# Kernel optimization log

Hardware: AMD Instinct MI355X
Metric: run time of the kernel (lower is better)

The kernel has to match this reference:

```python
import jax, jax.numpy as jnp
import numpy as np

N_NODES = 262144
N_EDGES = 4194304
N_GRAPHS = 1024


def setup_inputs() -> dict:
    key = jax.random.key(0)
    ks = jax.random.split(key, 12)
    inp = {}
    inp["x"] = jax.random.normal(ks[0], (N_NODES, 4), dtype=jnp.float32)
    inp["pos"] = jax.random.normal(ks[1], (N_NODES, 3), dtype=jnp.float32)
    # EquiLayer MLP: Linear(9,16) -> SiLU -> Linear(16,16); stored as (in,out)
    inp["W1"] = jax.random.normal(ks[2], (9, 16), dtype=jnp.float32) * (1.0 / np.sqrt(9))
    inp["b1"] = jnp.zeros((16,), dtype=jnp.float32)
    inp["W2"] = jax.random.normal(ks[3], (16, 16), dtype=jnp.float32) * 0.25
    inp["b2"] = jnp.zeros((16,), dtype=jnp.float32)
    # pool: Linear(16, k=2)
    inp["Wp"] = jax.random.normal(ks[4], (16, 2), dtype=jnp.float32) * 0.25
    inp["bp"] = jnp.zeros((2,), dtype=jnp.float32)
    # to_z: Linear(k*16=32, k*d=8)
    inp["Wz"] = jax.random.normal(ks[5], (32, 8), dtype=jnp.float32) * (1.0 / np.sqrt(32))
    inp["bz"] = jnp.zeros((8,), dtype=jnp.float32)
    inp["edge_index"] = jax.random.randint(ks[6], (2, N_EDGES), 0, N_NODES, dtype=jnp.int64)
    inp["batch"] = jnp.sort(jax.random.randint(ks[7], (N_NODES,), 0, N_GRAPHS, dtype=jnp.int64))
    return inp


def reference(x, pos, W1, b1, W2, b2, Wp, bp, Wz, bz, edge_index, batch):
    src = edge_index[0]  # x_j / source nodes
    dst = edge_index[1]  # x_i / target nodes (aggregation index, PyG default flow)
    n = x.shape[0]
    g = N_GRAPHS

    # edge distance feature: ||pos[src] - pos[dst]||  -> [E,1]
    rel = pos[src] - pos[dst]
    dist = jnp.sqrt(jnp.sum(rel * rel, axis=-1, keepdims=True))

    # message MLP on gathered endpoints: concat([x_i, x_j, dist]) -> [E,9]
    m_in = jnp.concatenate([x[dst], x[src], dist], axis=-1)
    h1 = jax.nn.silu(m_in @ W1 + b1)
    msg = h1 @ W2 + b2  # [E,16]

    # scatter-mean aggregation over target nodes
    msum = jax.ops.segment_sum(msg, dst, num_segments=n)
    cnt = jax.ops.segment_sum(jnp.ones((msg.shape[0], 1), msg.dtype), dst, num_segments=n)
    agg = msum / jnp.maximum(cnt, 1.0)

    h = jax.nn.relu(agg)  # [N,16]
    s = jax.nn.softmax(h @ Wp + bp, axis=-1)  # [N,k]

    # softmax-weighted scatter-sum pooling per graph: [G,k,16]
    pooled = jax.ops.segment_sum(s[:, :, None] * h[:, None, :], batch, num_segments=g)
    z = pooled.reshape(g, -1) @ Wz + bz  # [G, k*d]
    return z, s
```

## Files before the change

kernel.cpp:

```cpp
#include <hip/hip_runtime.h>
#include <hip/hip_fp16.h>
#include <math.h>

#define N_NODES 262144
#define N_EDGES 4194304
#define N_GRAPHS 1024
#define NBK 512
#define CAP 8960
#define ABLK 512
#define AEPB (N_EDGES / ABLK)

typedef _Float16 half2v __attribute__((ext_vector_type(2)));
__device__ inline half2v u2h(unsigned u) { union { unsigned u; half2v h; } c; c.u = u; return c.h; }
__device__ inline unsigned packh2(float a, float b) {
    union { __half2 h; unsigned u; } c; c.h = __floats2half2_rn(a, b); return c.u;
}

__global__ __launch_bounds__(256) void fusedAB(
    const int* __restrict__ ei, const float* __restrict__ x,
    const float* __restrict__ pos, int* __restrict__ gcur,
    int* __restrict__ binned, uint4* __restrict__ px16,
    float* __restrict__ pooled)
{
    __shared__ int lh2[2][NBK];
    int t = threadIdx.x, b = blockIdx.x;
    int half = (t >> 6) & 1;

    #pragma unroll
    for (int k = 0; k < 2; ++k) {
        int n = b * 512 + k * 256 + t;
        float4 v = ((const float4*)x)[n];
        float p0 = pos[3 * n], p1 = pos[3 * n + 1], p2 = pos[3 * n + 2];
        uint4 r;
        r.x = packh2(v.x, v.y);
        r.y = packh2(v.z, v.w);
        r.z = packh2(p0, p1);
        r.w = packh2(p2, 0.0f);
        px16[n] = r;
    }
    int pid = b * 256 + t;
    if (pid < 1025 * 32) pooled[pid] = 0.0f;

    #pragma unroll
    for (int k = 0; k < 2; ++k) {
        lh2[0][t + 256 * k] = 0;
        lh2[1][t + 256 * k] = 0;
    }
    __syncthreads();

    const int4* dsts = (const int4*)(ei + N_EDGES + b * AEPB);
    #pragma unroll
    for (int i = 0; i < AEPB / 1024; ++i) {
        int4 d4 = dsts[i * 256 + t];
        atomicAdd(&lh2[half][d4.x >> 9], 1);
        atomicAdd(&lh2[half][d4.y >> 9], 1);
        atomicAdd(&lh2[half][d4.z >> 9], 1);
        atomicAdd(&lh2[half][d4.w >> 9], 1);
    }
    __syncthreads();
    #pragma unroll
    for (int k = 0; k < 2; ++k) {
        int kb = t + 256 * k;
        int tot = lh2[0][kb] + lh2[1][kb];
        lh2[0][kb] = atomicAdd(&gcur[kb * 16], tot);
    }
    __syncthreads();
    const int4* srcp = (const int4*)(ei + b * AEPB);
    #pragma unroll
    for (int i = 0; i < AEPB / 1024; ++i) {
        int4 s4 = srcp[i * 256 + t];
        int4 d4 = dsts[i * 256 + t];
        int slot;
        slot = atomicAdd(&lh2[0][d4.x >> 9], 1);
        if (slot < CAP) binned[(size_t)(d4.x >> 9) * CAP + slot] = s4.x | ((d4.x & 511) << 18);
        slot = atomicAdd(&lh2[0][d4.y >> 9], 1);
        if (slot < CAP) binned[(size_t)(d4.y >> 9) * CAP + slot] = s4.y | ((d4.y & 511) << 18);
        slot = atomicAdd(&lh2[0][d4.z >> 9], 1);
        if (slot < CAP) binned[(size_t)(d4.z >> 9) * CAP + slot] = s4.z | ((d4.z & 511) << 18);
        slot = atomicAdd(&lh2[0][d4.w >> 9], 1);
        if (slot < CAP) binned[(size_t)(d4.w >> 9) * CAP + slot] = s4.w | ((d4.w & 511) << 18);
    }
}

__global__ __launch_bounds__(512) void passC_sort(
    const int* __restrict__ gcur,
    int* __restrict__ binned,
    int4* __restrict__ ndesc)
{
    __shared__ int lbuf[CAP];
    __shared__ int ldeg[512], lcur[512];
    __shared__ int wsum[8];
    int t = threadIdx.x, k = blockIdx.x;
    int ebase = k * CAP;
    int cnt = gcur[k * 16];
    if (cnt > CAP) cnt = CAP;

    ldeg[t] = 0;
    __syncthreads();
    for (int i = t; i < cnt; i += 512) {
        int pk = binned[ebase + i];
        lbuf[i] = pk;
        atomicAdd(&ldeg[pk >> 18], 1);
    }
    __syncthreads();
    int dgv = ldeg[t];

    int lane = t & 63, wid = t >> 6;
    int sv = dgv;
    #pragma unroll
    for (int o = 1; o < 64; o <<= 1) {
        int u = __shfl_up(sv, o);
        if (lane >= o) sv += u;
    }
    if (lane == 63) wsum[wid] = sv;
    __syncthreads();
    int pref = 0;
    #pragma unroll
    for (int w = 0; w < 8; ++w) pref += (w < wid) ? wsum[w] : 0;
    int excl = sv + pref - dgv;

    int n = k * 512 + t;
    lcur[t] = excl;

    int wbase = t & ~15;
    int rank = 0;
    #pragma unroll
    for (int j = 0; j < 16; ++j) {
        int dj = ldeg[wbase + j];
        rank += (dj < dgv) || (dj == dgv && (wbase + j) < t);
    }
    ndesc[(k << 9) + wbase + rank] = make_int4(ebase + excl, dgv, n, 0);
    __syncthreads();
    for (int i = t; i < cnt; i += 512) {
        int pk = lbuf[i];
        int sl = atomicAdd(&lcur[pk >> 18], 1);
        binned[ebase + sl] = pk & 0x3FFFF;
    }
}

__global__ __launch_bounds__(256) void node_gather_fused(
    const uint4* __restrict__ px16,
    const int* __restrict__ srcs, const int4* __restrict__ ndesc,
    const float* __restrict__ W1, const float* __restrict__ b1,
    const float* __restrict__ W2, const float* __restrict__ b2,
    const float* __restrict__ Wp, const float* __restrict__ bp,
    const int* __restrict__ batch,
    float* __restrict__ out_s, float* __restrict__ pooled)
{
    __shared__ uint4 sepk[16][17];
    __shared__ float smh[16][20];

    int t = threadIdx.x;
    int g = t & 15;
    int grp = t >> 4;
    int4 nd = ndesc[blockIdx.x * 16 + grp];
    int base = nd.x, dg = nd.y, n = nd.z;

    float w1c0 = W1[0 * 16 + g], w1c1 = W1[1 * 16 + g];
    float w1c2 = W1[2 * 16 + g], w1c3 = W1[3 * 16 + g];
    half2v wh45, wh67;
    wh45[0] = (_Float16)W1[4 * 16 + g];
    wh45[1] = (_Float16)W1[5 * 16 + g];
    wh67[0] = (_Float16)W1[6 * 16 + g];
    wh67[1] = (_Float16)W1[7 * 16 + g];
    float w1c8 = W1[8 * 16 + g];
    float b1g = b1[g], b2g = b2[g];
    float w2col[16];
    #pragma unroll
    for (int i = 0; i < 16; ++i) w2col[i] = W2[i * 16 + g];
    float wp0 = Wp[2 * g], wp1 = Wp[2 * g + 1];

    uint4 rn = px16[n];
    float2 f01 = __half22float2(*(__half2*)&rn.x);
    float2 f23 = __half22float2(*(__half2*)&rn.y);
    float2 f45 = __half22float2(*(__half2*)&rn.z);
    float2 f67 = __half22float2(*(__half2*)&rn.w);
    float pnx = f45.x, pny = f45.y, pnz = f67.x;
    float pre = b1g + f01.x * w1c0 + f01.y * w1c1 + f23.x * w1c2 + f23.y * w1c3;

    float sumH = 0.0f;

    int sC = 0, sN, sNN;
    if (g < dg) sC = srcs[base + g];
    sN = sC;
    if (16 + g < dg) sN = srcs[base + 16 + g];
    sNN = sN;
    if (32 + g < dg) sNN = srcs[base + 32 + g];
    uint4 rC = px16[sC];
    uint4 rN = px16[sN];

    for (int k0 = 0; k0 < dg; k0 += 16) {
        int rem = dg - k0;
        int cnt = rem < 16 ? rem : 16;
        if (g < cnt) {
            float2 e45 = __half22float2(*(__half2*)&rC.z);
            float2 e67 = __half22float2(*(__half2*)&rC.w);
            float dx = e45.x - pnx, dy = e45.y - pny, dz = e67.x - pnz;
            float dist = sqrtf(dx * dx + dy * dy + dz * dz);
            sepk[grp][g] = make_uint4(rC.x, rC.y, __float_as_uint(dist), 0u);
        }
        uint4 rNN = px16[sNN];
        int sNNN = sNN;
        if (k0 + 48 + g < dg) sNNN = srcs[base + k0 + 48 + g];
        int j = 0;
        for (; j + 1 < cnt; j += 2) {
            uint4 A = sepk[grp][j];
            uint4 B = sepk[grp][j + 1];
            float a = fmaf(__uint_as_float(A.z), w1c8, pre);
            a = __builtin_amdgcn_fdot2(u2h(A.x), wh45, a, false);
            a = __builtin_amdgcn_fdot2(u2h(A.y), wh67, a, false);
            sumH += a * __builtin_amdgcn_rcpf(1.0f + __expf(-a));
            float b = fmaf(__uint_as_float(B.z), w1c8, pre);
            b = __builtin_amdgcn_fdot2(u2h(B.x), wh45, b, false);
            b = __builtin_amdgcn_fdot2(u2h(B.y), wh67, b, false);
            sumH += b * __builtin_amdgcn_rcpf(1.0f + __expf(-b));
        }
        if (j < cnt) {
            uint4 A = sepk[grp][j];
            float a = fmaf(__uint_as_float(A.z), w1c8, pre);
            a = __builtin_amdgcn_fdot2(u2h(A.x), wh45, a, false);
            a = __builtin_amdgcn_fdot2(u2h(A.y), wh67, a, false);
            sumH += a * __builtin_amdgcn_rcpf(1.0f + __expf(-a));
        }
        rC = rN; rN = rNN; sNN = sNNN;
    }

    smh[grp][g] = sumH;
    float4 s0v = *(const float4*)&smh[grp][0];
    float4 s1v = *(const float4*)&smh[grp][4];
    float4 s2v = *(const float4*)&smh[grp][8];
    float4 s3v = *(const float4*)&smh[grp][12];
    float red = s0v.x * w2col[0] + s0v.y * w2col[1] + s0v.z * w2col[2] + s0v.w * w2col[3]
              + s1v.x * w2col[4] + s1v.y * w2col[5] + s1v.z * w2col[6] + s1v.w * w2col[7]
              + s2v.x * w2col[8] + s2v.y * w2col[9] + s2v.z * w2col[10] + s2v.w * w2col[11]
              + s3v.x * w2col[12] + s3v.y * w2col[13] + s3v.z * w2col[14] + s3v.w * w2col[15];

    float fdg = (float)dg;
    float inv = 1.0f / fmaxf(fdg, 1.0f);
    float h = fmaxf((red + fdg * b2g) * inv, 0.0f);

    float c0 = h * wp0, c1 = h * wp1;
    #pragma unroll
    for (int mset = 8; mset > 0; mset >>= 1) {
        c0 += __shfl_xor(c0, mset);
        c1 += __shfl_xor(c1, mset);
    }
    float l0 = c0 + bp[0], l1 = c1 + bp[1];
    float mx = fmaxf(l0, l1);
    float e0s = __expf(l0 - mx), e1s = __expf(l1 - mx);
    float isum = 1.0f / (e0s + e1s);
    float s0 = e0s * isum, s1 = e1s * isum;

    if (g == 0) ((float2*)out_s)[n] = make_float2(s0, s1);

    __shared__ float lpool[2][32];
    __shared__ int sg0;
    if (t == 0) sg0 = batch[blockIdx.x * 16];
    if (t < 64) lpool[t >> 5][t & 31] = 0.0f;
    __syncthreads();

    int gid = batch[n];
    int idx = gid - sg0;
    float p0 = s0 * h, p1 = s1 * h;
    if (idx < 2) {
        atomicAdd(&lpool[idx][g], p0);
        atomicAdd(&lpool[idx][16 + g], p1);
    } else {
        atomicAdd(&pooled[gid * 32 + g], p0);
        atomicAdd(&pooled[gid * 32 + 16 + g], p1);
    }
    __syncthreads();
    if (t < 32) {
        float v = lpool[0][t];
        if (v != 0.0f) atomicAdd(&pooled[sg0 * 32 + t], v);
        v = lpool[1][t];
        if (v != 0.0f) atomicAdd(&pooled[(sg0 + 1) * 32 + t], v);
    }
}

__global__ __launch_bounds__(256) void z_kernel(const float* __restrict__ pooled,
                                                const float* __restrict__ Wz,
                                                const float* __restrict__ bz,
                                                float* __restrict__ out_z) {
    int idx = blockIdx.x * 256 + threadIdx.x;
    if (idx >= N_GRAPHS * 8) return;
    int gph = idx >> 3, o = idx & 7;
    float a = bz[o];
    const float* pp = pooled + (size_t)gph * 32;
    #pragma unroll
    for (int j = 0; j < 32; ++j) a = fmaf(pp[j], Wz[j * 8 + o], a);
    out_z[idx] = a;
}

extern "C" void kernel_launch(void* const* d_in, const int* in_sizes, int n_in,
                              void* d_out, int out_size, void* d_ws, size_t ws_size,
                              hipStream_t stream) {
    const float* x    = (const float*)d_in[0];
    const float* pos  = (const float*)d_in[1];
    const float* W1   = (const float*)d_in[2];
    const float* b1   = (const float*)d_in[3];
    const float* W2   = (const float*)d_in[4];
    const float* b2   = (const float*)d_in[5];
    const float* Wp   = (const float*)d_in[6];
    const float* bp   = (const float*)d_in[7];
    const float* Wz   = (const float*)d_in[8];
    const float* bz   = (const float*)d_in[9];
    const int*   ei   = (const int*)d_in[10];
    const int*   batch= (const int*)d_in[11];
    float* out = (float*)d_out;
    float* out_z = out;
    float* out_s = out + N_GRAPHS * 8;

    int* gcur     = (int*)d_ws;
    int* binned   = gcur + NBK * 16;
    int4* ndesc   = (int4*)(binned + (size_t)NBK * CAP);
    float* pooled = (float*)(ndesc + N_NODES);
    uint4* px16   = (uint4*)(pooled + 1025 * 32);

    hipMemsetAsync(gcur, 0, NBK * 16 * sizeof(int), stream);
    fusedAB<<<ABLK, 256, 0, stream>>>(ei, x, pos, gcur, binned, px16, pooled);
    passC_sort<<<NBK, 512, 0, stream>>>(gcur, binned, ndesc);
    node_gather_fused<<<N_NODES / 16, 256, 0, stream>>>(
        px16, binned, ndesc, W1, b1, W2, b2, Wp, bp, batch, out_s, pooled);
    z_kernel<<<32, 256, 0, stream>>>(pooled, Wz, bz, out_z);
}
```

Before: 173.9 us.

## Fuse bucket sort and node gather into one per-bucket kernel using LDS

Merges the per-bucket counting sort and the per-node message/aggregation kernel into a single kernel with one block per 512-node bucket. The sorted source lists, offsets, degree permutation and batch ids stay in shared memory, so the global write-back of sorted sources, the ndesc array and one launch are dropped. Each 16-lane group now processes 16 nodes in sequence, and graph pooling is reduced locally over up to 8 graphs per block. In exchange there are only 512 blocks with large LDS use (~50KB), which lowers occupancy and latency hiding for the random px16 gathers, and the prefetch depth drops from two chunks ahead to one.

```diff
diff --git a/kernel.cpp b/kernel.cpp
--- a/kernel.cpp
+++ b/kernel.cpp
@@ -82,79 +82,85 @@
     }
 }
 
-__global__ __launch_bounds__(512) void passC_sort(
-    const int* __restrict__ gcur,
-    int* __restrict__ binned,
-    int4* __restrict__ ndesc)
-{
-    __shared__ int lbuf[CAP];
-    __shared__ int ldeg[512], lcur[512];
-    __shared__ int wsum[8];
-    int t = threadIdx.x, k = blockIdx.x;
-    int ebase = k * CAP;
-    int cnt = gcur[k * 16];
-    if (cnt > CAP) cnt = CAP;
-
-    ldeg[t] = 0;
-    __syncthreads();
-    for (int i = t; i < cnt; i += 512) {
-        int pk = binned[ebase + i];
-        lbuf[i] = pk;
-        atomicAdd(&ldeg[pk >> 18], 1);
-    }
-    __syncthreads();
-    int dgv = ldeg[t];
-
-    int lane = t & 63, wid = t >> 6;
-    int sv = dgv;
-    #pragma unroll
-    for (int o = 1; o < 64; o <<= 1) {
-        int u = __shfl_up(sv, o);
-        if (lane >= o) sv += u;
-    }
-    if (lane == 63) wsum[wid] = sv;
-    __syncthreads();
-    int pref = 0;
-    #pragma unroll
-    for (int w = 0; w < 8; ++w) pref += (w < wid) ? wsum[w] : 0;
-    int excl = sv + pref - dgv;
-
-    int n = k * 512 + t;
-    lcur[t] = excl;
-
-    int wbase = t & ~15;
-    int rank = 0;
-    #pragma unroll
-    for (int j = 0; j < 16; ++j) {
-        int dj = ldeg[wbase + j];
-        rank += (dj < dgv) || (dj == dgv && (wbase + j) < t);
-    }
-    ndesc[(k << 9) + wbase + rank] = make_int4(ebase + excl, dgv, n, 0);
-    __syncthreads();
-    for (int i = t; i < cnt; i += 512) {
-        int pk = lbuf[i];
-        int sl = atomicAdd(&lcur[pk >> 18], 1);
-        binned[ebase + sl] = pk & 0x3FFFF;
-    }
-}
-
-__global__ __launch_bounds__(256) void node_gather_fused(
+__global__ __launch_bounds__(512) void bucket_fused(
+    const int* __restrict__ gcur, const int* __restrict__ binned,
     const uint4* __restrict__ px16,
-    const int* __restrict__ srcs, const int4* __restrict__ ndesc,
     const float* __restrict__ W1, const float* __restrict__ b1,
     const float* __restrict__ W2, const float* __restrict__ b2,
     const float* __restrict__ Wp, const float* __restrict__ bp,
     const int* __restrict__ batch,
     float* __restrict__ out_s, float* __restrict__ pooled)
 {
-    __shared__ uint4 sepk[16][17];
-    __shared__ float smh[16][20];
-
-    int t = threadIdx.x;
-    int g = t & 15;
-    int grp = t >> 4;
-    int4 nd = ndesc[blockIdx.x * 16 + grp];
-    int base = nd.x, dg = nd.y, n = nd.z;
+    __shared__ int lbuf[CAP];
+    __shared__ int ldegs[512], lstart[512], lcur[512], lperm[512];
+    __shared__ int bloc[512];
+    __shared__ int wsum[8];
+    __shared__ uint4 sepk[32][17];
+    __shared__ float smh[32][20];
+    __shared__ float lpool[8][33];
+
+    int t = threadIdx.x, k = blockIdx.x;
+    int ebase = k * CAP;
+    int cnt = gcur[k * 16];
+    if (cnt > CAP) cnt = CAP;
+
+    ldegs[t] = 0;
+    bloc[t] = batch[(k << 9) + t];
+    for (int i = t; i < 8 * 33; i += 512) ((float*)lpool)[i] = 0.0f;
+    __syncthreads();
+
+    for (int i = t; i < cnt; i += 512) {
+        int pk = binned[ebase + i];
+        lbuf[i] = pk;
+        atomicAdd(&ldegs[pk >> 18], 1);
+    }
+    __syncthreads();
+    int dgv = ldegs[t];
+
+    int lane = t & 63, wid = t >> 6;
+    int sv = dgv;
+    #pragma unroll
+    for (int o = 1; o < 64; o <<= 1) {
+        int u = __shfl_up(sv, o);
+        if (lane >= o) sv += u;
+    }
+    if (lane == 63) wsum[wid] = sv;
+    __syncthreads();
+    int pref = 0;
+    #pragma unroll
+    for (int w = 0; w < 8; ++w) pref += (w < wid) ? wsum[w] : 0;
+    int excl = sv + pref - dgv;
+    lstart[t] = excl;
+    lcur[t] = excl;
+
+    int wbase = t & ~15;
+    int rank = 0;
+    #pragma unroll
+    for (int j = 0; j < 16; ++j) {
+        int dj = ldegs[wbase + j];
+        rank += (dj < dgv) || (dj == dgv && (wbase + j) < t);
+    }
+    lperm[wbase + rank] = t;
+    __syncthreads();
+
+    int regpk[18];
+    #pragma unroll
+    for (int c = 0; c < 18; ++c) {
+        int i = t + c * 512;
+        regpk[c] = (i < cnt) ? lbuf[i] : -1;
+    }
+    __syncthreads();
+    #pragma unroll
+    for (int c = 0; c < 18; ++c) {
+        int pk = regpk[c];
+        if (pk >= 0) {
+            int sl = atomicAdd(&lcur[pk >> 18], 1);
+            lbuf[sl] = pk & 0x3FFFF;
+        }
+    }
+    __syncthreads();
+
+    int g = t & 15, grp = t >> 4;
 
     float w1c0 = W1[0 * 16 + g], w1c1 = W1[1 * 16 + g];
     float w1c2 = W1[2 * 16 + g], w1c3 = W1[3 * 16 + g];
@@ -169,112 +175,112 @@
     #pragma unroll
     for (int i = 0; i < 16; ++i) w2col[i] = W2[i * 16 + g];
     float wp0 = Wp[2 * g], wp1 = Wp[2 * g + 1];
-
-    uint4 rn = px16[n];
-    float2 f01 = __half22float2(*(__half2*)&rn.x);
-    float2 f23 = __half22float2(*(__half2*)&rn.y);
-    float2 f45 = __half22float2(*(__half2*)&rn.z);
-    float2 f67 = __half22float2(*(__half2*)&rn.w);
-    float pnx = f45.x, pny = f45.y, pnz = f67.x;
-    float pre = b1g + f01.x * w1c0 + f01.y * w1c1 + f23.x * w1c2 + f23.y * w1c3;
-
-    float sumH = 0.0f;
-
-    int sC = 0, sN, sNN;
-    if (g < dg) sC = srcs[base + g];
-    sN = sC;
-    if (16 + g < dg) sN = srcs[base + 16 + g];
-    sNN = sN;
-    if (32 + g < dg) sNN = srcs[base + 32 + g];
-    uint4 rC = px16[sC];
-    uint4 rN = px16[sN];
-
-    for (int k0 = 0; k0 < dg; k0 += 16) {
-        int rem = dg - k0;
-        int cnt = rem < 16 ? rem : 16;
-        if (g < cnt) {
-            float2 e45 = __half22float2(*(__half2*)&rC.z);
-            float2 e67 = __half22float2(*(__half2*)&rC.w);
-            float dx = e45.x - pnx, dy = e45.y - pny, dz = e67.x - pnz;
-            float dist = sqrtf(dx * dx + dy * dy + dz * dz);
-            sepk[grp][g] = make_uint4(rC.x, rC.y, __float_as_uint(dist), 0u);
-        }
-        uint4 rNN = px16[sNN];
-        int sNNN = sNN;
-        if (k0 + 48 + g < dg) sNNN = srcs[base + k0 + 48 + g];
-        int j = 0;
-        for (; j + 1 < cnt; j += 2) {
-            uint4 A = sepk[grp][j];
-            uint4 B = sepk[grp][j + 1];
-            float a = fmaf(__uint_as_float(A.z), w1c8, pre);
-            a = __builtin_amdgcn_fdot2(u2h(A.x), wh45, a, false);
-            a = __builtin_amdgcn_fdot2(u2h(A.y), wh67, a, false);
-            sumH += a * __builtin_amdgcn_rcpf(1.0f + __expf(-a));
-            float b = fmaf(__uint_as_float(B.z), w1c8, pre);
-            b = __builtin_amdgcn_fdot2(u2h(B.x), wh45, b, false);
-            b = __builtin_amdgcn_fdot2(u2h(B.y), wh67, b, false);
-            sumH += b * __builtin_amdgcn_rcpf(1.0f + __expf(-b));
-        }
-        if (j < cnt) {
-            uint4 A = sepk[grp][j];
-            float a = fmaf(__uint_as_float(A.z), w1c8, pre);
-            a = __builtin_amdgcn_fdot2(u2h(A.x), wh45, a, false);
-            a = __builtin_amdgcn_fdot2(u2h(A.y), wh67, a, false);
-            sumH += a * __builtin_amdgcn_rcpf(1.0f + __expf(-a));
-        }
-        rC = rN; rN = rNN; sNN = sNNN;
-    }
-
-    smh[grp][g] = sumH;
-    float4 s0v = *(const float4*)&smh[grp][0];
-    float4 s1v = *(const float4*)&smh[grp][4];
-    float4 s2v = *(const float4*)&smh[grp][8];
-    float4 s3v = *(const float4*)&smh[grp][12];
-    float red = s0v.x * w2col[0] + s0v.y * w2col[1] + s0v.z * w2col[2] + s0v.w * w2col[3]
-              + s1v.x * w2col[4] + s1v.y * w2col[5] + s1v.z * w2col[6] + s1v.w * w2col[7]
-              + s2v.x * w2col[8] + s2v.y * w2col[9] + s2v.z * w2col[10] + s2v.w * w2col[11]
-              + s3v.x * w2col[12] + s3v.y * w2col[13] + s3v.z * w2col[14] + s3v.w * w2col[15];
-
-    float fdg = (float)dg;
-    float inv = 1.0f / fmaxf(fdg, 1.0f);
-    float h = fmaxf((red + fdg * b2g) * inv, 0.0f);
-
-    float c0 = h * wp0, c1 = h * wp1;
-    #pragma unroll
-    for (int mset = 8; mset > 0; mset >>= 1) {
-        c0 += __shfl_xor(c0, mset);
-        c1 += __shfl_xor(c1, mset);
-    }
-    float l0 = c0 + bp[0], l1 = c1 + bp[1];
-    float mx = fmaxf(l0, l1);
-    float e0s = __expf(l0 - mx), e1s = __expf(l1 - mx);
-    float isum = 1.0f / (e0s + e1s);
-    float s0 = e0s * isum, s1 = e1s * isum;
-
-    if (g == 0) ((float2*)out_s)[n] = make_float2(s0, s1);
-
-    __shared__ float lpool[2][32];
-    __shared__ int sg0;
-    if (t == 0) sg0 = batch[blockIdx.x * 16];
-    if (t < 64) lpool[t >> 5][t & 31] = 0.0f;
-    __syncthreads();
-
-    int gid = batch[n];
-    int idx = gid - sg0;
-    float p0 = s0 * h, p1 = s1 * h;
-    if (idx < 2) {
-        atomicAdd(&lpool[idx][g], p0);
-        atomicAdd(&lpool[idx][16 + g], p1);
-    } else {
-        atomicAdd(&pooled[gid * 32 + g], p0);
-        atomicAdd(&pooled[gid * 32 + 16 + g], p1);
-    }
-    __syncthreads();
-    if (t < 32) {
-        float v = lpool[0][t];
-        if (v != 0.0f) atomicAdd(&pooled[sg0 * 32 + t], v);
-        v = lpool[1][t];
-        if (v != 0.0f) atomicAdd(&pooled[(sg0 + 1) * 32 + t], v);
+    int sg0 = bloc[0];
+
+    for (int nn = 0; nn < 16; ++nn) {
+        int w = lperm[grp * 16 + nn];
+        int n = (k << 9) + w;
+        int base = lstart[w];
+        int dg = ldegs[w];
+
+        uint4 rn = px16[n];
+        float2 f01 = __half22float2(*(__half2*)&rn.x);
+        float2 f23 = __half22float2(*(__half2*)&rn.y);
+        float2 f45 = __half22float2(*(__half2*)&rn.z);
+        float2 f67 = __half22float2(*(__half2*)&rn.w);
+        float pnx = f45.x, pny = f45.y, pnz = f67.x;
+        float pre = b1g + f01.x * w1c0 + f01.y * w1c1 + f23.x * w1c2 + f23.y * w1c3;
+
+        float sumH = 0.0f;
+
+        int sC = (g < dg) ? lbuf[base + g] : 0;
+        uint4 rC = px16[sC];
+        int sN = (16 + g < dg) ? lbuf[base + 16 + g] : sC;
+
+        for (int k0 = 0; k0 < dg; k0 += 16) {
+            int rem = dg - k0;
+            int cc = rem < 16 ? rem : 16;
+            if (g < cc) {
+                float2 e45 = __half22float2(*(__half2*)&rC.z);
+                float2 e67 = __half22float2(*(__half2*)&rC.w);
+                float dx = e45.x - pnx, dy = e45.y - pny, dz = e67.x - pnz;
+                float dist = sqrtf(dx * dx + dy * dy + dz * dz);
+                sepk[grp][g] = make_uint4(rC.x, rC.y, __float_as_uint(dist), 0u);
+            }
+            uint4 rNext = px16[sN];
+            int sNN = (k0 + 32 + g < dg) ? lbuf[base + k0 + 32 + g] : sN;
+            int j = 0;
+            for (; j + 1 < cc; j += 2) {
+                uint4 A = sepk[grp][j];
+                uint4 B = sepk[grp][j + 1];
+                float a = fmaf(__uint_as_float(A.z), w1c8, pre);
+                a = __builtin_amdgcn_fdot2(u2h(A.x), wh45, a, false);
+                a = __builtin_amdgcn_fdot2(u2h(A.y), wh67, a, false);
+                sumH += a * __builtin_amdgcn_rcpf(1.0f + __expf(-a));
+                float bb = fmaf(__uint_as_float(B.z), w1c8, pre);
+                bb = __builtin_amdgcn_fdot2(u2h(B.x), wh45, bb, false);
+                bb = __builtin_amdgcn_fdot2(u2h(B.y), wh67, bb, false);
+                sumH += bb * __builtin_amdgcn_rcpf(1.0f + __expf(-bb));
+            }
+            if (j < cc) {
+                uint4 A = sepk[grp][j];
+                float a = fmaf(__uint_as_float(A.z), w1c8, pre);
+                a = __builtin_amdgcn_fdot2(u2h(A.x), wh45, a, false);
+                a = __builtin_amdgcn_fdot2(u2h(A.y), wh67, a, false);
+                sumH += a * __builtin_amdgcn_rcpf(1.0f + __expf(-a));
+            }
+            rC = rNext;
+            sN = sNN;
+        }
+
+        smh[grp][g] = sumH;
+        float4 s0v = *(const float4*)&smh[grp][0];
+        float4 s1v = *(const float4*)&smh[grp][4];
+        float4 s2v = *(const float4*)&smh[grp][8];
+        float4 s3v = *(const float4*)&smh[grp][12];
+        float red = s0v.x * w2col[0] + s0v.y * w2col[1] + s0v.z * w2col[2] + s0v.w * w2col[3]
+                  + s1v.x * w2col[4] + s1v.y * w2col[5] + s1v.z * w2col[6] + s1v.w * w2col[7]
+                  + s2v.x * w2col[8] + s2v.y * w2col[9] + s2v.z * w2col[10] + s2v.w * w2col[11]
+                  + s3v.x * w2col[12] + s3v.y * w2col[13] + s3v.z * w2col[14] + s3v.w * w2col[15];
+
+        float fdg = (float)dg;
+        float inv = 1.0f / fmaxf(fdg, 1.0f);
+        float h = fmaxf((red + fdg * b2g) * inv, 0.0f);
+
+        float c0 = h * wp0, c1 = h * wp1;
+        #pragma unroll
+        for (int mset = 8; mset > 0; mset >>= 1) {
+            c0 += __shfl_xor(c0, mset);
+            c1 += __shfl_xor(c1, mset);
+        }
+        float l0 = c0 + bp[0], l1 = c1 + bp[1];
+        float mx = fmaxf(l0, l1);
+        float e0s = __expf(l0 - mx), e1s = __expf(l1 - mx);
+        float isum = 1.0f / (e0s + e1s);
+        float s0 = e0s * isum, s1 = e1s * isum;
+
+        if (g == 0) ((float2*)out_s)[n] = make_float2(s0, s1);
+
+        int gid = bloc[w];
+        int idx = gid - sg0;
+        float p0 = s0 * h, p1 = s1 * h;
+        if (idx < 8) {
+            atomicAdd(&lpool[idx][g], p0);
+            atomicAdd(&lpool[idx][16 + g], p1);
+        } else {
+            atomicAdd(&pooled[gid * 32 + g], p0);
+            atomicAdd(&pooled[gid * 32 + 16 + g], p1);
+        }
+    }
+    __syncthreads();
+
+    if (t < 256) {
+        int gi = t >> 5, c = t & 31;
+        int ngr = bloc[511] - sg0 + 1;
+        if (gi < ngr && gi < 8) {
+            float v = lpool[gi][c];
+            if (v != 0.0f) atomicAdd(&pooled[(sg0 + gi) * 32 + c], v);
+        }
     }
 }
 
@@ -313,14 +319,12 @@
 
     int* gcur     = (int*)d_ws;
     int* binned   = gcur + NBK * 16;
-    int4* ndesc   = (int4*)(binned + (size_t)NBK * CAP);
-    float* pooled = (float*)(ndesc + N_NODES);
+    float* pooled = (float*)(binned + (size_t)NBK * CAP);
     uint4* px16   = (uint4*)(pooled + 1025 * 32);
 
     hipMemsetAsync(gcur, 0, NBK * 16 * sizeof(int), stream);
     fusedAB<<<ABLK, 256, 0, stream>>>(ei, x, pos, gcur, binned, px16, pooled);
-    passC_sort<<<NBK, 512, 0, stream>>>(gcur, binned, ndesc);
-    node_gather_fused<<<N_NODES / 16, 256, 0, stream>>>(
-        px16, binned, ndesc, W1, b1, W2, b2, Wp, bp, batch, out_s, pooled);
+    bucket_fused<<<NBK, 512, 0, stream>>>(gcur, binned, px16, W1, b1, W2, b2,
+                                          Wp, bp, batch, out_s, pooled);
     z_kernel<<<32, 256, 0, stream>>>(pooled, Wz, bz, out_z);
 }
```

Result: faster. 159.1 us (-8.5%).
